# Performance work log

Hardware: AMD Instinct MI355X
Metric: run time of the kernel (lower is better)

## Reference

```python
import jax, jax.numpy as jnp
import numpy as np

LMAX = 6
F_IN, F_OUT = 64, 64
N_ROT = 64  # n_angles**3
IRREP_FLAT = sum((2 * l + 1) ** 2 for l in range(LMAX + 1))  # 455
BATCH = 1024


def setup_inputs() -> dict:
    key = jax.random.key(0)
    k_x, k_d, k_w = jax.random.split(key, 3)
    x = jax.random.normal(k_x, (BATCH, F_IN, IRREP_FLAT), dtype=jnp.float32)
    D = jax.random.normal(k_d, (N_ROT, IRREP_FLAT), dtype=jnp.float32)  # flat Wigner-D buffer
    w = jax.random.normal(k_w, (F_IN, F_OUT, N_ROT), dtype=jnp.float32)
    return {"x": x, "D": D, "w": w}


def reference(x, D, w):
    B, f_in, _ = x.shape
    f_out = w.shape[1]
    n_rot = D.shape[0]
    # psi[f,g,i] = sum_n D[n,i] * w[f,g,n] / sqrt(N)
    psi = jnp.einsum('ni,fgn->fgi', D, w) / jnp.sqrt(jnp.asarray(n_rot, x.dtype))
    outs = []
    off = 0
    for l in range(LMAX + 1):
        d = 2 * l + 1          # irrep dim == multiplicity for so3_irreps
        blk = d * d
        # weight block: (f_in, f_out, mul_in=u, mul_out=v)
        Wl = psi[:, :, off:off + blk].reshape(f_in, f_out, d, d)
        # input block: (B, f_in, mul=u, irrep_dim=m)
        xl = x[:, :, off:off + blk].reshape(B, f_in, d, d)
        # e3nn Linear path norm ('element'): 1/sqrt(f_in * mul_in)
        norm = 1.0 / np.sqrt(f_in * d)
        yl = jnp.einsum('bfum,fguv->bgvm', xl, Wl) * norm
        outs.append(yl.reshape(B, f_out, blk))
        off += blk
    return jnp.concatenate(outs, axis=-1)  # (B, f_out, 455)
```

## Files before the change

### kernel.cpp

```cpp
#include <hip/hip_runtime.h>
#include <stdint.h>


typedef __bf16 bf16x8 __attribute__((ext_vector_type(8)));
typedef float floatx4 __attribute__((ext_vector_type(4)));

#define XROW 29120

__device__ __forceinline__ unsigned short f2bf(float f) {
  union { float f; unsigned int u; } c; c.f = f;
  unsigned int u = c.u;
  return (unsigned short)((u + 0x7FFFu + ((u >> 16) & 1u)) >> 16);
}
__device__ __forceinline__ unsigned int pack2(float a, float b) {
  return (unsigned int)f2bf(a) | ((unsigned int)f2bf(b) << 16);
}

__host__ __device__ constexpr int d_of(int L) { return 2 * L + 1; }
__host__ __device__ constexpr int off_of(int L) { int s = 0; for (int i = 0; i < L; ++i) s += d_of(i) * d_of(i); return s; }
__host__ __device__ constexpr size_t a_off(int L) { size_t s = 0; for (int i = 0; i < L; ++i) s += (size_t)65536 * d_of(i) * d_of(i); return s; }
__host__ __device__ constexpr size_t b_off(int L) { size_t s = a_off(7); for (int i = 0; i < L; ++i) s += (size_t)4096 * d_of(i) * (d_of(i) + 1); return s; }

__global__ __launch_bounds__(256) void prep(const float* __restrict__ x, const float* __restrict__ Dm,
                                            const float* __restrict__ w, unsigned short* __restrict__ ws) {
  __shared__ __align__(16) float smem[64 * 68 + 64 * 172];
  const int tid = threadIdx.x;
  const int bid = blockIdx.x;

  if (bid < 448) {
    float* wg = smem;
    float* Dl = smem + 64 * 68;
    const int g = bid & 63, l = bid >> 6;
    const int d = 2 * l + 1, d2 = d * d, K = 64 * d;
    int off = 0; size_t boff = a_off(7);
    for (int i = 0; i < l; ++i) { int dd = 2 * i + 1; off += dd * dd; boff += (size_t)4096 * dd * (dd + 1); }
    unsigned short* B = ws + boff;

    for (int t = tid; t < 4096; t += 256) {
      int n = t & 63, f = t >> 6;
      wg[n * 68 + f] = w[(size_t)f * 4096 + g * 64 + n];
    }
    for (int t = tid; t < 64 * 172; t += 256) {
      int n = t / 172, r = t - n * 172;
      Dl[t] = (r < d2) ? Dm[n * 455 + off + r] : 0.f;
    }
    __syncthreads();

    const float sl = 1.0f / (64.0f * sqrtf((float)d));
    const int RT = (d2 + 3) >> 2;
    for (int tt = tid; tt < 16 * RT; tt += 256) {
      const int ft = tt & 15, rt = tt >> 4;
      float acc[4][4] = {};
      for (int n = 0; n < 64; ++n) {
        floatx4 wv = *(const floatx4*)(wg + n * 68 + ft * 4);
        floatx4 dv = *(const floatx4*)(Dl + n * 172 + rt * 4);
#pragma unroll
        for (int a = 0; a < 4; ++a)
#pragma unroll
          for (int b2 = 0; b2 < 4; ++b2) acc[a][b2] += wv[a] * dv[b2];
      }
#pragma unroll
      for (int b2 = 0; b2 < 4; ++b2) {
        int r = rt * 4 + b2;
        if (r < d2) {
          int u = r / d, v = r - u * d;
          size_t base = (size_t)(g * d + v) * K + u * 64 + ft * 4;
#pragma unroll
          for (int a = 0; a < 4; ++a) B[base + a] = f2bf(acc[a][b2] * sl);
        }
      }
    }
    {
      int nn = 64 * d + g;
      for (int k = tid; k < K; k += 256) B[(size_t)nn * K + k] = 0;
    }
  } else {
    float* xs = smem;
    const int b = bid - 448;
    const float* xb = x + (size_t)b * XROW;
    size_t aoff = 0;

    for (int t = tid; t < 64 * 165; t += 256) { int f = t / 165, c = t - f * 165; xs[t] = xb[(size_t)f * 455 + c]; }
    __syncthreads();
    int off = 0;
#pragma unroll
    for (int l = 0; l < 5; ++l) {
      const int d = 2 * l + 1, d2 = d * d, n1 = 64 * d2;
      unsigned int* A = (unsigned int*)(ws + aoff + (size_t)b * n1);
      for (int t = tid; t < (n1 >> 1); t += 256) {
        int f2 = t & 31, s = t >> 5;
        int u = s % d, m = s / d;
        int c = off + u * d + m;
        A[t] = pack2(xs[(2 * f2) * 165 + c], xs[(2 * f2 + 1) * 165 + c]);
      }
      off += d2; aoff += (size_t)1024 * n1;
    }
    __syncthreads();
    for (int t = tid; t < 64 * 121; t += 256) { int f = t / 121, c = t - f * 121; xs[t] = xb[(size_t)f * 455 + 165 + c]; }
    __syncthreads();
    {
      const int n1 = 64 * 121;
      unsigned int* A = (unsigned int*)(ws + aoff + (size_t)b * n1);
      for (int t = tid; t < (n1 >> 1); t += 256) {
        int f2 = t & 31, s = t >> 5;
        int u = s % 11, m = s / 11;
        int c = u * 11 + m;
        A[t] = pack2(xs[(2 * f2) * 121 + c], xs[(2 * f2 + 1) * 121 + c]);
      }
      aoff += (size_t)1024 * n1;
    }
    __syncthreads();
    for (int t = tid; t < 64 * 169; t += 256) { int f = t / 169, c = t - f * 169; xs[t] = xb[(size_t)f * 455 + 286 + c]; }
    __syncthreads();
    {
      const int n1 = 64 * 169;
      unsigned int* A = (unsigned int*)(ws + aoff + (size_t)b * n1);
      for (int t = tid; t < (n1 >> 1); t += 256) {
        int f2 = t & 31, s = t >> 5;
        int u = s % 13, m = s / 13;
        int c = u * 13 + m;
        A[t] = pack2(xs[(2 * f2) * 169 + c], xs[(2 * f2 + 1) * 169 + c]);
      }
    }
  }
}

__device__ __forceinline__ void async_copy16(const void* gp, void* lp) {
  __builtin_amdgcn_global_load_lds((__attribute__((address_space(1))) void*)gp,
                                   (__attribute__((address_space(3))) void*)lp, 16, 0, 0);
}

template <int L>
__device__ __forceinline__ void gemm_body(int local, const unsigned short* __restrict__ ws,
                                          float* __restrict__ out,
                                          unsigned short* As, unsigned short* Bs) {
  constexpr int d = 2 * L + 1;
  constexpr int K = 64 * d;
  constexpr int NT = (d + 1) / 2;
  constexpr int OFF = off_of(L);
  constexpr int KT = 2 * d;
  const unsigned short* A = ws + a_off(L);
  const unsigned short* B = ws + b_off(L);
  const int x8 = local & 7, tt = local >> 3;
  const int mt = (tt / NT) * 8 + x8;
  const int nt = tt % NT;
  const int tid = threadIdx.x;
  const int w = tid >> 6, ln = tid & 63;
  const int wm = w >> 1, wn = w & 1;
  const int q = ln >> 4, r16 = ln & 15;

  const unsigned short* gp[4];
  unsigned short* ldst[4];
#pragma unroll
  for (int i = 0; i < 4; ++i) {
    int c = i * 256 + tid;
    if (i < 2) {
      int row = c >> 2, ch = (c & 3) ^ ((c >> 3) & 3);
      gp[i] = A + (size_t)(mt * 128 + row) * K + ch * 8;
      ldst[i] = As + (i * 256 + w * 64) * 8;
    } else {
      int c2 = c - 512;
      int row = c2 >> 2, ch = (c2 & 3) ^ ((c2 >> 3) & 3);
      gp[i] = B + (size_t)(nt * 128 + row) * K + ch * 8;
      ldst[i] = Bs + ((i - 2) * 256 + w * 64) * 8;
    }
  }

  const int sq = q ^ ((r16 >> 1) & 3);
  const int aoffs0 = (wm * 64 + r16) * 32 + sq * 8;
  const int boffs0 = (wn * 64 + r16) * 32 + sq * 8;

  floatx4 acc[4][4] = {};

#pragma unroll
  for (int i = 0; i < 4; ++i) { async_copy16(gp[i], ldst[i]); gp[i] += 32; }
  __syncthreads();

  int cur = 0;
  for (int kt = 0; kt < KT; ++kt) {
    if (kt + 1 < KT) {
      const int nb = (cur ^ 1) * 4096;
#pragma unroll
      for (int i = 0; i < 4; ++i) { async_copy16(gp[i], ldst[i] + nb); gp[i] += 32; }
    }
    const unsigned short* Asc = As + cur * 4096;
    const unsigned short* Bsc = Bs + cur * 4096;
    bf16x8 af[4], bfr[4];
#pragma unroll
    for (int mi = 0; mi < 4; ++mi) af[mi] = *(const bf16x8*)(Asc + aoffs0 + mi * 512);
#pragma unroll
    for (int ni = 0; ni < 4; ++ni) bfr[ni] = *(const bf16x8*)(Bsc + boffs0 + ni * 512);
#pragma unroll
    for (int mi = 0; mi < 4; ++mi)
#pragma unroll
      for (int ni = 0; ni < 4; ++ni)
        acc[mi][ni] = __builtin_amdgcn_mfma_f32_16x16x32_bf16(af[mi], bfr[ni], acc[mi][ni], 0, 0, 0);
    __syncthreads();
    cur ^= 1;
  }

#pragma unroll
  for (int ni = 0; ni < 4; ++ni) {
    int Cc = nt * 128 + wn * 64 + ni * 16 + r16;
    if (Cc < 64 * d) {
      int g = Cc / d, v = Cc - (Cc / d) * d;
#pragma unroll
      for (int mi = 0; mi < 4; ++mi) {
        int R0 = mt * 128 + wm * 64 + mi * 16 + q * 4;
#pragma unroll
        for (int reg = 0; reg < 4; ++reg) {
          int R = R0 + reg;
          int bb = R / d, m = R - (R / d) * d;
          out[(size_t)bb * XROW + g * 455 + OFF + v * d + m] = acc[mi][ni][reg];
        }
      }
    }
  }
}

__global__ __launch_bounds__(256) void gemm_all(const unsigned short* __restrict__ ws, float* __restrict__ out) {
  __shared__ alignas(16) unsigned short As[2 * 128 * 32];
  __shared__ alignas(16) unsigned short Bs[2 * 128 * 32];
  int b0 = 2015 - (int)blockIdx.x;
  if      (b0 <    8) gemm_body<0>(b0,        ws, out, As, Bs);
  else if (b0 <   56) gemm_body<1>(b0 -    8, ws, out, As, Bs);
  else if (b0 <  176) gemm_body<2>(b0 -   56, ws, out, As, Bs);
  else if (b0 <  400) gemm_body<3>(b0 -  176, ws, out, As, Bs);
  else if (b0 <  760) gemm_body<4>(b0 -  400, ws, out, As, Bs);
  else if (b0 < 1288) gemm_body<5>(b0 -  760, ws, out, As, Bs);
  else                gemm_body<6>(b0 - 1288, ws, out, As, Bs);
}

extern "C" void kernel_launch(void* const* d_in, const int* in_sizes, int n_in,
                              void* d_out, int out_size, void* d_ws, size_t ws_size,
                              hipStream_t stream) {
  const float* x = (const float*)d_in[0];
  const float* D = (const float*)d_in[1];
  const float* w = (const float*)d_in[2];
  float* out = (float*)d_out;
  unsigned short* ws = (unsigned short*)d_ws;

  hipLaunchKernelGGL(prep, dim3(1472), dim3(256), 0, stream, x, D, w, ws);
  hipLaunchKernelGGL(gemm_all, dim3(2016), dim3(256), 0, stream, ws, out);
}
```

Measured before the change: 369.9 us.

## Triple-buffer LDS tiles with explicit vmcnt waits in GEMM main loop

Replaces the double-buffered async global-to-LDS pipeline with a three-stage ring buffer. Loads are issued two tiles ahead, and per-stage s_waitcnt vmcnt counts replace the full __syncthreads. The loop is fully unrolled with sched barriers so MFMA work overlaps more outstanding memory traffic. LDS use grows from 32KB to 48KB per block, which may reduce occupancy, and the code now depends on hand-tuned wait counts being correct.

```diff
diff --git a/kernel.cpp b/kernel.cpp
--- a/kernel.cpp
+++ b/kernel.cpp
@@ -128,6 +128,15 @@
 __device__ __forceinline__ void async_copy16(const void* gp, void* lp) {
   __builtin_amdgcn_global_load_lds((__attribute__((address_space(1))) void*)gp,
                                    (__attribute__((address_space(3))) void*)lp, 16, 0, 0);
+}
+
+template <int N>
+__device__ __forceinline__ void wait_vmcnt() {
+  asm volatile("s_waitcnt vmcnt(%0)" :: "n"(N) : "memory");
+}
+__device__ __forceinline__ void wait_lgkm0() {
+  asm volatile("s_waitcnt lgkmcnt(0)" ::: "memory");
+  __builtin_amdgcn_sched_barrier(0);
 }
 
 template <int L>
@@ -173,30 +182,44 @@
   floatx4 acc[4][4] = {};
 
 #pragma unroll
-  for (int i = 0; i < 4; ++i) { async_copy16(gp[i], ldst[i]); gp[i] += 32; }
-  __syncthreads();
-
-  int cur = 0;
+  for (int t = 0; t < 3; ++t) {
+    if (t < KT) {
+#pragma unroll
+      for (int i = 0; i < 4; ++i) { async_copy16(gp[i], ldst[i] + t * 4096); gp[i] += 32; }
+    }
+  }
+
+#pragma unroll
   for (int kt = 0; kt < KT; ++kt) {
-    if (kt + 1 < KT) {
-      const int nb = (cur ^ 1) * 4096;
-#pragma unroll
-      for (int i = 0; i < 4; ++i) { async_copy16(gp[i], ldst[i] + nb); gp[i] += 32; }
-    }
-    const unsigned short* Asc = As + cur * 4096;
-    const unsigned short* Bsc = Bs + cur * 4096;
+    wait_lgkm0();
+    if (KT - 1 - kt >= 2)      wait_vmcnt<8>();
+    else if (KT - 1 - kt == 1) wait_vmcnt<4>();
+    else                       wait_vmcnt<0>();
+    __builtin_amdgcn_sched_barrier(0);
+    __builtin_amdgcn_s_barrier();
+    __builtin_amdgcn_sched_barrier(0);
+
+    const unsigned short* Asc = As + (kt % 3) * 4096;
+    const unsigned short* Bsc = Bs + (kt % 3) * 4096;
     bf16x8 af[4], bfr[4];
 #pragma unroll
     for (int mi = 0; mi < 4; ++mi) af[mi] = *(const bf16x8*)(Asc + aoffs0 + mi * 512);
 #pragma unroll
     for (int ni = 0; ni < 4; ++ni) bfr[ni] = *(const bf16x8*)(Bsc + boffs0 + ni * 512);
+
+    if (kt + 3 < KT) {
+      wait_lgkm0();
+      __builtin_amdgcn_s_barrier();
+      __builtin_amdgcn_sched_barrier(0);
+#pragma unroll
+      for (int i = 0; i < 4; ++i) { async_copy16(gp[i], ldst[i] + ((kt + 3) % 3) * 4096); gp[i] += 32; }
+    }
+
 #pragma unroll
     for (int mi = 0; mi < 4; ++mi)
 #pragma unroll
       for (int ni = 0; ni < 4; ++ni)
         acc[mi][ni] = __builtin_amdgcn_mfma_f32_16x16x32_bf16(af[mi], bfr[ni], acc[mi][ni], 0, 0, 0);
-    __syncthreads();
-    cur ^= 1;
   }
 
 #pragma unroll
@@ -219,8 +242,8 @@
 }
 
 __global__ __launch_bounds__(256) void gemm_all(const unsigned short* __restrict__ ws, float* __restrict__ out) {
-  __shared__ alignas(16) unsigned short As[2 * 128 * 32];
-  __shared__ alignas(16) unsigned short Bs[2 * 128 * 32];
+  __shared__ alignas(16) unsigned short As[3 * 128 * 32];
+  __shared__ alignas(16) unsigned short Bs[3 * 128 * 32];
   int b0 = 2015 - (int)blockIdx.x;
   if      (b0 <    8) gemm_body<0>(b0,        ws, out, As, Bs);
   else if (b0 <   56) gemm_body<1>(b0 -    8, ws, out, As, Bs);
```

Result: faster. 354.3 us (-4.2%).
